# Optimization experiments

Hardware: AMD Instinct MI355X
Metric: run time of the kernel (lower is better)

## Reference

```python
import jax, jax.numpy as jnp
import numpy as np

T = 4096
HIDDEN = 2048
N_HEADS = 16
N_KV_HEADS = 4
HEAD_DIM = 128
WINDOW = 1024  # per_layer_sliding_window = WINDOW + 1 -> q attends keys with q_pos - k_pos <= WINDOW
ROPE_THETA = 100000.0
QKV_OUT = (N_HEADS + 2 * N_KV_HEADS) * HEAD_DIM  # 3072


def setup_inputs() -> dict:
    key = jax.random.key(0)
    k1, k2, k3, k4 = jax.random.split(key, 4)
    return {
        "hidden_states": jax.random.normal(k1, (T, HIDDEN), dtype=jnp.float32),
        "positions": jnp.arange(T, dtype=jnp.int32),
        "w_qkv": jax.random.normal(k2, (HIDDEN, QKV_OUT), dtype=jnp.float32) * 0.02,
        "b_qkv": jax.random.normal(k3, (QKV_OUT,), dtype=jnp.float32) * 0.02,
        "w_o": jax.random.normal(k4, (N_HEADS * HEAD_DIM, HIDDEN), dtype=jnp.float32) * 0.02,
    }


def _apply_rope(x, positions):
    # x: [T, n_heads, HEAD_DIM], neox-style rotary over full head dim
    half = HEAD_DIM // 2
    inv_freq = 1.0 / (ROPE_THETA ** (jnp.arange(half, dtype=jnp.float32) / half))
    freqs = positions.astype(jnp.float32)[:, None] * inv_freq[None, :]  # [T, half]
    cos = jnp.cos(freqs)[:, None, :]  # [T, 1, half]
    sin = jnp.sin(freqs)[:, None, :]
    x1, x2 = x[..., :half], x[..., half:]
    return jnp.concatenate([x1 * cos - x2 * sin, x2 * cos + x1 * sin], axis=-1)


def reference(hidden_states, positions, w_qkv, b_qkv, w_o):
    # QKV projection (bias=True)
    qkv = hidden_states @ w_qkv + b_qkv  # [T, QKV_OUT]
    q_size = N_HEADS * HEAD_DIM
    kv_size = N_KV_HEADS * HEAD_DIM
    q = qkv[:, :q_size].reshape(T, N_HEADS, HEAD_DIM)
    k = qkv[:, q_size:q_size + kv_size].reshape(T, N_KV_HEADS, HEAD_DIM)
    v = qkv[:, q_size + kv_size:].reshape(T, N_KV_HEADS, HEAD_DIM)

    # RoPE on q and k
    q = _apply_rope(q, positions)
    k = _apply_rope(k, positions)

    # GQA: expand kv heads to match query heads
    group = N_HEADS // N_KV_HEADS
    k = jnp.repeat(k, group, axis=1)  # [T, N_HEADS, HEAD_DIM]
    v = jnp.repeat(v, group, axis=1)

    scale = HEAD_DIM ** -0.5
    scores = jnp.einsum('qhd,khd->hqk', q, k) * scale  # [H, T, T]

    # causal + sliding-window mask: j <= i and i - j <= WINDOW
    i = jnp.arange(T)[:, None]
    j = jnp.arange(T)[None, :]
    mask = (j <= i) & (i - j <= WINDOW)  # [T, T]
    scores = jnp.where(mask[None, :, :], scores, jnp.finfo(scores.dtype).min)

    probs = jax.nn.softmax(scores, axis=-1)
    attn = jnp.einsum('hqk,khd->qhd', probs, v)  # [T, H, HEAD_DIM]
    attn = attn.reshape(T, N_HEADS * HEAD_DIM)

    # output projection (bias=False)
    return attn @ w_o
```

## Files before the change

kernel.cpp:

```cpp
#include <hip/hip_runtime.h>
#include <cstdint>

#define T_TOK 4096
#define HID 2048
#define NH 16
#define NKV 4
#define HD 128
#define WIN 1024
#define QKVO 3072

typedef float f32x4 __attribute__((ext_vector_type(4)));
typedef float f32x16 __attribute__((ext_vector_type(16)));
typedef __bf16 bf16x8 __attribute__((ext_vector_type(8)));
typedef __bf16 bf16x4 __attribute__((ext_vector_type(4)));
typedef unsigned int u32x4 __attribute__((ext_vector_type(4)));

__device__ __forceinline__ void gload16(const void* g, void* lds) {
  auto gp = reinterpret_cast<__attribute__((address_space(1))) void*>(
      reinterpret_cast<uintptr_t>(g));
  auto lp = reinterpret_cast<__attribute__((address_space(3))) void*>(
      reinterpret_cast<uintptr_t>(lds));
  __builtin_amdgcn_global_load_lds(gp, lp, 16, 0, 0);
}

__device__ __forceinline__ f32x4 mfma16(bf16x8 a, bf16x8 b, f32x4 c) {
  return __builtin_amdgcn_mfma_f32_16x16x32_bf16(a, b, c, 0, 0, 0);
}
__device__ __forceinline__ f32x16 mfma32(bf16x8 a, bf16x8 b, f32x16 c) {
  return __builtin_amdgcn_mfma_f32_32x32x16_bf16(a, b, c, 0, 0, 0);
}
__device__ __forceinline__ unsigned cvtpk(float lo, float hi) {
  unsigned r;
  asm("v_cvt_pk_bf16_f32 %0, %1, %2" : "=v"(r) : "v"(lo), "v"(hi));
  return r;
}
__device__ __forceinline__ void pl32swap(unsigned& a, unsigned& b) {
  asm volatile("v_permlane32_swap_b32 %0, %1" : "+v"(a), "+v"(b));
}

__global__ __launch_bounds__(256) void k_f32_to_bf16(const float* __restrict__ x,
                                                     __bf16* __restrict__ y) {
  const size_t e = (size_t)blockIdx.x * 256 + threadIdx.x;
  const float4* xv = (const float4*)x;
  float4 a = xv[e * 2], b = xv[e * 2 + 1];
  bf16x8 o;
  o[0] = (__bf16)a.x; o[1] = (__bf16)a.y; o[2] = (__bf16)a.z; o[3] = (__bf16)a.w;
  o[4] = (__bf16)b.x; o[5] = (__bf16)b.y; o[6] = (__bf16)b.z; o[7] = (__bf16)b.w;
  *(bf16x8*)(y + e * 8) = o;
}

__global__ __launch_bounds__(256) void k_transpose2(
    const float* __restrict__ W1, __bf16* __restrict__ Wt1,
    const float* __restrict__ W2, __bf16* __restrict__ Wt2) {
  __shared__ float lt[64][69];
  int bid = blockIdx.x;
  const float* W;
  __bf16* Wt;
  int R, C;
  if (bid < 1536) {
    W = W1; Wt = Wt1; R = HID; C = QKVO;
  } else {
    bid -= 1536; W = W2; Wt = Wt2; R = HID; C = HID;
  }
  const int nbx = C >> 6;
  const int c0 = (bid % nbx) << 6;
  const int r0 = (bid / nbx) << 6;
  const int tid = threadIdx.x;
  const int tx = tid & 15, ty = tid >> 4;
#pragma unroll
  for (int i = 0; i < 4; i++) {
    const int r = ty + 16 * i;
    const float4 v = *(const float4*)(W + (size_t)(r0 + r) * C + c0 + 4 * tx);
    lt[r][4 * tx] = v.x;
    lt[r][4 * tx + 1] = v.y;
    lt[r][4 * tx + 2] = v.z;
    lt[r][4 * tx + 3] = v.w;
  }
  __syncthreads();
  const int ux = tid & 7, uy = tid >> 3;
#pragma unroll
  for (int i = 0; i < 2; i++) {
    const int c = uy + 32 * i;
    bf16x8 o;
#pragma unroll
    for (int k = 0; k < 8; k++) o[k] = (__bf16)lt[8 * ux + k][c];
    *(bf16x8*)(Wt + (size_t)(c0 + c) * R + r0 + 8 * ux) = o;
  }
}

__global__ void k_rope_tab(const int* __restrict__ pos, float* __restrict__ cosT,
                           float* __restrict__ sinT) {
  const int t = blockIdx.x;
  const int d = threadIdx.x;
  const float inv = exp2f(-(float)d * (16.609640474436812f / 64.0f));
  const float fr = (float)pos[t] * inv;
  cosT[t * 64 + d] = cosf(fr);
  sinT[t * 64 + d] = sinf(fr);
}

template <int MODE>
__global__ __launch_bounds__(256, 2) void k_gemm(
    const __bf16* __restrict__ A, const __bf16* __restrict__ Bt,
    const float* __restrict__ bias, float* __restrict__ C,
    const float* __restrict__ cosT, const float* __restrict__ sinT,
    __bf16* __restrict__ Qp, __bf16* __restrict__ Kp, __bf16* __restrict__ Vf,
    int M, int N, int K) {
  __shared__ __align__(16) __bf16 smem[32768];
  const int tid = threadIdx.x;
  const int lane = tid & 63;
  const int w = tid >> 6;
  const int wr = w >> 1, wc = w & 1;
  const int c = lane & 15, g = lane >> 4;
  const int csw = (c & 7) << 4;

  const int nstc = N >> 9;
  const int bid = blockIdx.x;
  const int xcd = bid & 7;
  const int j = bid >> 3;
  const int spx = (int)(gridDim.x >> 7);
  const int s = xcd * spx + (j >> 4);
  const int q = j & 15;
  const int by = (s / nstc) * 4 + (q >> 2);
  const int bx = (s % nstc) * 4 + (q & 3);
  const int m0 = by << 7, n0 = bx << 7;

  const int o0 = w * 4096 + lane * 16;
  const int srow = 32 * w + (lane >> 3);
  const int schunk = (lane & 7) ^ ((lane >> 3) & 7);
  const __bf16* gA0 = A + (size_t)(m0 + srow) * K + schunk * 8;
  const __bf16* gB0 = Bt + (size_t)(n0 + srow) * K + schunk * 8;

  f32x4 acc[4][4] = {};

  {
    char* la = (char*)smem;
    char* lb = (char*)smem + 32768;
#pragma unroll
    for (int qq = 0; qq < 4; qq++) {
      gload16(gA0 + (size_t)qq * 8 * K, la + o0 + qq * 1024);
      gload16(gB0 + (size_t)qq * 8 * K, lb + o0 + qq * 1024);
    }
  }
  __syncthreads();

  int cur = 0;
  for (int kt = 0; kt < K; kt += 64) {
    if (kt + 64 < K) {
      char* la = (char*)smem + (cur ^ 1) * 16384;
      char* lb = (char*)smem + 32768 + (cur ^ 1) * 16384;
#pragma unroll
      for (int qq = 0; qq < 4; qq++) {
        gload16(gA0 + kt + 64 + (size_t)qq * 8 * K, la + o0 + qq * 1024);
        gload16(gB0 + kt + 64 + (size_t)qq * 8 * K, lb + o0 + qq * 1024);
      }
    }
    const char* as = (const char*)smem + cur * 16384;
    const char* bs = (const char*)smem + 32768 + cur * 16384;
#pragma unroll
    for (int ds = 0; ds < 2; ds++) {
      bf16x8 af[4], bfr[4];
#pragma unroll
      for (int mi = 0; mi < 4; mi++)
        af[mi] = *(const bf16x8*)(as + (wr * 64 + mi * 16 + c) * 128 +
                                  ((ds * 64 + g * 16) ^ csw));
#pragma unroll
      for (int ni = 0; ni < 4; ni++)
        bfr[ni] = *(const bf16x8*)(bs + (wc * 64 + ni * 16 + c) * 128 +
                                   ((ds * 64 + g * 16) ^ csw));
#pragma unroll
      for (int mi = 0; mi < 4; mi++)
#pragma unroll
        for (int ni = 0; ni < 4; ni++)
          acc[mi][ni] = mfma16(af[mi], bfr[ni], acc[mi][ni]);
    }
    __syncthreads();
    cur ^= 1;
  }

  if constexpr (MODE == 0) {
#pragma unroll
    for (int ni = 0; ni < 4; ni++) {
      const int col = n0 + wc * 64 + ni * 16 + c;
#pragma unroll
      for (int mi = 0; mi < 4; mi++)
#pragma unroll
        for (int r = 0; r < 4; r++) {
          const int row = m0 + wr * 64 + mi * 16 + 4 * g + r;
          C[(size_t)row * N + col] = acc[mi][ni][r];
        }
    }
  } else {
    __bf16* sm = smem;
#pragma unroll
    for (int ni = 0; ni < 4; ni++) {
      const int col = wc * 64 + ni * 16 + c;
      const float bv = bias[n0 + col];
#pragma unroll
      for (int mi = 0; mi < 4; mi++)
#pragma unroll
        for (int r = 0; r < 4; r++)
          sm[(wr * 64 + mi * 16 + 4 * g + r) * 136 + col] =
              (__bf16)(acc[mi][ni][r] + bv);
    }
    __syncthreads();

    if (n0 < (NH + NKV) * HD) {
      const bool isq = n0 < NH * HD;
      const float sc = isq ? (0.08838834764831845f * 1.4426950408889634f) : 1.0f;
      __bf16* base = isq ? (Qp + (size_t)(n0 >> 7) * T_TOK * HD)
                         : (Kp + (size_t)((n0 >> 7) - NH) * T_TOK * HD);
#pragma unroll
      for (int jj = 0; jj < 4; jj++) {
        const int e = jj * 256 + tid;
        const int tl = e >> 3, ch = e & 7;
        const int tt = m0 + tl;
        const bf16x8 x1 = *(const bf16x8*)(sm + tl * 136 + ch * 8);
        const bf16x8 x2 = *(const bf16x8*)(sm + tl * 136 + 64 + ch * 8);
        const float4 c0 = *(const float4*)(cosT + tt * 64 + ch * 8);
        const float4 c1 = *(const float4*)(cosT + tt * 64 + ch * 8 + 4);
        const float4 s0 = *(const float4*)(sinT + tt * 64 + ch * 8);
        const float4 s1 = *(const float4*)(sinT + tt * 64 + ch * 8 + 4);
        const float cs[8] = {c0.x, c0.y, c0.z, c0.w, c1.x, c1.y, c1.z, c1.w};
        const float sn[8] = {s0.x, s0.y, s0.z, s0.w, s1.x, s1.y, s1.z, s1.w};
        bf16x8 o1, o2;
#pragma unroll
        for (int i = 0; i < 8; i++) {
          const float a = (float)x1[i], b = (float)x2[i];
          o1[i] = (__bf16)((a * cs[i] - b * sn[i]) * sc);
          o2[i] = (__bf16)((b * cs[i] + a * sn[i]) * sc);
        }
        const int d2s = isq ? ch * 8 : ((ch * 8) ^ ((tt & 7) << 3));
        __bf16* dst = base + (size_t)tt * HD;
        *(bf16x8*)(dst + d2s) = o1;
        *(bf16x8*)(dst + 64 + d2s) = o2;
      }
    } else {
      const int kv = (n0 >> 7) - (NH + NKV);
#pragma unroll
      for (int st2 = 0; st2 < 2; st2++) {
        __bf16* outb = Vf + ((size_t)kv * 64 + (m0 >> 6) + st2) * 8192;
#pragma unroll
        for (int jj = 0; jj < 4; jj++) {
          const int u = jj * 256 + tid;
          const int lu = u & 63, ks = (u >> 6) & 3, mq = u >> 8;
          const int d = mq * 32 + (lu & 31);
          const int tb = st2 * 64 + ks * 16 + ((lu >> 5) << 3);
          bf16x8 o;
#pragma unroll
          for (int jz = 0; jz < 8; jz++) o[jz] = sm[(tb + jz) * 136 + d];
          *(bf16x8*)(outb + (size_t)u * 8) = o;
        }
      }
    }
  }
}

__global__ __launch_bounds__(256, 2) void k_attn(const __bf16* __restrict__ Qp,
                                                 const __bf16* __restrict__ Kp,
                                                 const __bf16* __restrict__ Vf,
                                                 __bf16* __restrict__ attnO) {
  __shared__ __align__(16) __bf16 Ks[2][64 * 128];

  const int tid = threadIdx.x;
  const int lane = tid & 63;
  const int w = tid >> 6;
  const int l31 = lane & 31;
  const int hi = lane >> 5;
  const int swz = (lane & 7) << 4;
  const int bid = blockIdx.x;
  const int xcd = bid & 7, j = bid >> 3;
  const int h = ((xcd >> 1) << 2) + ((xcd & 1) << 1) + (j & 1);
  const int qb = 31 - (j >> 1);
  const int kvh = h >> 2;
  const int q0 = qb * 128;
  const int iw = q0 + 32 * w;
  const int irow = iw + l31;

  bf16x8 qf[8];
  {
    const __bf16* qbase = Qp + ((size_t)h * T_TOK + irow) * HD;
#pragma unroll
    for (int ds = 0; ds < 8; ds++)
      qf[ds] = *(const bf16x8*)(qbase + ds * 16 + hi * 8);
  }

  f32x16 ot[4] = {};
  float mrun = 0.0f, lrun = 0.0f;

  const int jstart = (q0 >= WIN) ? (q0 - WIN) : 0;
  const int niter = (q0 + 128 - jstart) >> 6;

  const char* Kg = (const char*)Kp + (size_t)kvh * T_TOK * HD * 2;
  const char* kg0 = Kg + (size_t)(jstart + 16 * w + (lane >> 4)) * 256 + (lane & 15) * 16;
  const __bf16* Vgb = Vf + (size_t)kvh * 64 * 8192;

#pragma unroll
  for (int q = 0; q < 4; q++)
    gload16(kg0 + q * 1024, (char*)&Ks[0][0] + w * 4096 + q * 1024);

  int cur = 0;

  for (int it = 0; it < niter; ++it) {
    const int j0 = jstart + it * 64;
    __syncthreads();

    if (it + 1 < niter) {
      const char* kg = kg0 + (size_t)(it + 1) * 16384;
      char* kd = (char*)&Ks[cur ^ 1][0] + w * 4096;
#pragma unroll
      for (int q = 0; q < 4; q++) gload16(kg + q * 1024, kd + q * 1024);
    }

    if (j0 > iw + 31) { cur ^= 1; continue; }
    if (iw - (j0 + 63) > WIN) { cur ^= 1; continue; }

    const __bf16* vt = Vgb + (size_t)(j0 >> 6) * 8192;
    bf16x8 vf[4][4];
#pragma unroll
    for (int m = 0; m < 4; m++)
#pragma unroll
      for (int ks = 0; ks < 4; ks++)
        vf[m][ks] = *(const bf16x8*)(vt + (m * 256 + ks * 64 + lane) * 8);

    const char* kb = (const char*)&Ks[cur][0];

    f32x16 st[2] = {};
    __builtin_amdgcn_s_setprio(1);
#pragma unroll
    for (int t = 0; t < 2; t++)
#pragma unroll
      for (int ds = 0; ds < 8; ds++) {
        bf16x8 kf = *(const bf16x8*)(kb + (t * 32 + l31) * 256 +
                                     ((ds * 32 + hi * 16) ^ swz));
        st[t] = mfma32(kf, qf[ds], st[t]);
      }
    __builtin_amdgcn_s_setprio(0);

    float p[2][16];
    float cmax = -1e30f;
    const bool interior = (j0 + 63 <= iw) && (iw + 31 - j0 <= WIN);
    if (interior) {
#pragma unroll
      for (int t = 0; t < 2; t++)
#pragma unroll
        for (int r = 0; r < 16; r++) {
          const float s = st[t][r];
          p[t][r] = s;
          cmax = fmaxf(cmax, s);
        }
    } else {
      const int jb = irow - j0 - 4 * hi;
#pragma unroll
      for (int t = 0; t < 2; t++)
#pragma unroll
        for (int r = 0; r < 16; r++) {
          float s = st[t][r];
          const int off = 32 * t + (r & 3) + 8 * (r >> 2);
          s = ((unsigned)(jb - off) <= WIN) ? s : -1e30f;
          p[t][r] = s;
          cmax = fmaxf(cmax, s);
        }
    }
    cmax = fmaxf(cmax, __shfl_xor(cmax, 32));

    if (!__all(cmax <= mrun + 11.54f)) {
      const float mn = fmaxf(mrun, cmax);
      const float alpha = exp2f(mrun - mn);
      lrun *= alpha;
#pragma unroll
      for (int m = 0; m < 4; m++) ot[m] *= alpha;
      mrun = mn;
    }
    float rs = 0.0f;
#pragma unroll
    for (int t = 0; t < 2; t++)
#pragma unroll
      for (int r = 0; r < 16; r++) {
        const float e_ = exp2f(p[t][r] - mrun);
        p[t][r] = e_;
        rs += e_;
      }
    rs += __shfl_xor(rs, 32);
    lrun += rs;

    bf16x8 pb[4];
#pragma unroll
    for (int t = 0; t < 2; t++) {
      unsigned wds[8];
#pragma unroll
      for (int i = 0; i < 8; i++) wds[i] = cvtpk(p[t][2 * i], p[t][2 * i + 1]);
      pl32swap(wds[0], wds[2]);
      pl32swap(wds[1], wds[3]);
      pl32swap(wds[4], wds[6]);
      pl32swap(wds[5], wds[7]);
      u32x4 f0 = {wds[0], wds[1], wds[2], wds[3]};
      u32x4 f1 = {wds[4], wds[5], wds[6], wds[7]};
      pb[2 * t] = __builtin_bit_cast(bf16x8, f0);
      pb[2 * t + 1] = __builtin_bit_cast(bf16x8, f1);
    }

    __builtin_amdgcn_s_setprio(1);
#pragma unroll
    for (int m = 0; m < 4; m++)
#pragma unroll
      for (int ks = 0; ks < 4; ks++)
        ot[m] = mfma32(vf[m][ks], pb[ks], ot[m]);
    __builtin_amdgcn_s_setprio(0);

    cur ^= 1;
  }

  const float inv_l = 1.0f / lrun;
  __bf16* orow = attnO + (size_t)irow * (NH * HD) + h * HD;
#pragma unroll
  for (int m = 0; m < 4; m++)
#pragma unroll
    for (int rg = 0; rg < 4; rg++) {
      const int d0 = 32 * m + 8 * rg + 4 * hi;
      bf16x4 o4;
#pragma unroll
      for (int r = 0; r < 4; r++) o4[r] = (__bf16)(ot[m][4 * rg + r] * inv_l);
      *(bf16x4*)(orow + d0) = o4;
    }
}

extern "C" void kernel_launch(void* const* d_in, const int* in_sizes, int n_in,
                              void* d_out, int out_size, void* d_ws, size_t ws_size,
                              hipStream_t stream) {
  (void)in_sizes; (void)n_in; (void)out_size; (void)ws_size;
  const float* hidden = (const float*)d_in[0];
  const int* positions = (const int*)d_in[1];
  const float* w_qkv = (const float*)d_in[2];
  const float* b_qkv = (const float*)d_in[3];
  const float* w_o = (const float*)d_in[4];
  float* out = (float*)d_out;

  char* ws = (char*)d_ws;
  __bf16* Hb = (__bf16*)ws;    ws += (size_t)T_TOK * HID * 2;
  __bf16* Wqkvt = (__bf16*)ws; ws += (size_t)QKVO * HID * 2;
  __bf16* Wot = (__bf16*)ws;   ws += (size_t)HID * HID * 2;
  float* cosT = (float*)ws;    ws += (size_t)T_TOK * 64 * 4;
  float* sinT = (float*)ws;    ws += (size_t)T_TOK * 64 * 4;
  __bf16* Qp = (__bf16*)ws;    ws += (size_t)NH * T_TOK * HD * 2;
  __bf16* Kp = (__bf16*)ws;    ws += (size_t)NKV * T_TOK * HD * 2;
  __bf16* Vfb = (__bf16*)ws;   ws += (size_t)NKV * 64 * 8192 * 2;
  __bf16* attnb = (__bf16*)ws; ws += (size_t)T_TOK * NH * HD * 2;

  k_f32_to_bf16<<<T_TOK * HID / (256 * 8), 256, 0, stream>>>(hidden, Hb);
  k_transpose2<<<2560, 256, 0, stream>>>(w_qkv, Wqkvt, w_o, Wot);
  k_rope_tab<<<T_TOK, 64, 0, stream>>>(positions, cosT, sinT);
  k_gemm<1><<<(T_TOK / 128) * (QKVO / 128), 256, 0, stream>>>(
      Hb, Wqkvt, b_qkv, nullptr, cosT, sinT, Qp, Kp, Vfb, T_TOK, QKVO, HID);
  k_attn<<<512, 256, 0, stream>>>(Qp, Kp, Vfb, attnb);
  k_gemm<0><<<(T_TOK / 128) * (HID / 128), 256, 0, stream>>>(
      attnb, Wot, nullptr, out, nullptr, nullptr, nullptr, nullptr, nullptr,
      T_TOK, HID, HID);
}
```

Measured before the change: 172.4 us.

## Store K in MFMA-fragment layout and load directly to registers in attention

The QKV GEMM epilogue now writes roped K into a pre-swizzled per-64-token fragment layout, the same way V is stored, so each lane's MFMA operand is one contiguous 16-byte load. The attention kernel drops the shared-memory K double buffer and its per-iteration barriers and reads K fragments straight from global/L2. Each wave also iterates only over its own 32-row key range instead of the block-wide range, which removes idle iterations. The cost is more global load traffic per wave, with no shared-memory reuse of K across the four waves, and higher register pressure from holding 16 K fragments.

```diff
diff --git a/kernel.cpp b/kernel.cpp
--- a/kernel.cpp
+++ b/kernel.cpp
@@ -103,7 +103,7 @@
     const __bf16* __restrict__ A, const __bf16* __restrict__ Bt,
     const float* __restrict__ bias, float* __restrict__ C,
     const float* __restrict__ cosT, const float* __restrict__ sinT,
-    __bf16* __restrict__ Qp, __bf16* __restrict__ Kp, __bf16* __restrict__ Vf,
+    __bf16* __restrict__ Qp, __bf16* __restrict__ Kf, __bf16* __restrict__ Vf,
     int M, int N, int K) {
   __shared__ __align__(16) __bf16 smem[32768];
   const int tid = threadIdx.x;
@@ -204,11 +204,9 @@
     }
     __syncthreads();
 
-    if (n0 < (NH + NKV) * HD) {
-      const bool isq = n0 < NH * HD;
-      const float sc = isq ? (0.08838834764831845f * 1.4426950408889634f) : 1.0f;
-      __bf16* base = isq ? (Qp + (size_t)(n0 >> 7) * T_TOK * HD)
-                         : (Kp + (size_t)((n0 >> 7) - NH) * T_TOK * HD);
+    if (n0 < NH * HD) {
+      const float sc = 0.08838834764831845f * 1.4426950408889634f;
+      __bf16* base = Qp + (size_t)(n0 >> 7) * T_TOK * HD;
 #pragma unroll
       for (int jj = 0; jj < 4; jj++) {
         const int e = jj * 256 + tid;
@@ -229,10 +227,49 @@
           o1[i] = (__bf16)((a * cs[i] - b * sn[i]) * sc);
           o2[i] = (__bf16)((b * cs[i] + a * sn[i]) * sc);
         }
-        const int d2s = isq ? ch * 8 : ((ch * 8) ^ ((tt & 7) << 3));
         __bf16* dst = base + (size_t)tt * HD;
-        *(bf16x8*)(dst + d2s) = o1;
-        *(bf16x8*)(dst + 64 + d2s) = o2;
+        *(bf16x8*)(dst + ch * 8) = o1;
+        *(bf16x8*)(dst + 64 + ch * 8) = o2;
+      }
+    } else if (n0 < (NH + NKV) * HD) {
+#pragma unroll
+      for (int jj = 0; jj < 4; jj++) {
+        const int e = jj * 256 + tid;
+        const int tl = e >> 3, ch = e & 7;
+        const int tt = m0 + tl;
+        const bf16x8 x1 = *(const bf16x8*)(sm + tl * 136 + ch * 8);
+        const bf16x8 x2 = *(const bf16x8*)(sm + tl * 136 + 64 + ch * 8);
+        const float4 c0 = *(const float4*)(cosT + tt * 64 + ch * 8);
+        const float4 c1 = *(const float4*)(cosT + tt * 64 + ch * 8 + 4);
+        const float4 s0 = *(const float4*)(sinT + tt * 64 + ch * 8);
+        const float4 s1 = *(const float4*)(sinT + tt * 64 + ch * 8 + 4);
+        const float cs[8] = {c0.x, c0.y, c0.z, c0.w, c1.x, c1.y, c1.z, c1.w};
+        const float sn[8] = {s0.x, s0.y, s0.z, s0.w, s1.x, s1.y, s1.z, s1.w};
+        bf16x8 o1, o2;
+#pragma unroll
+        for (int i = 0; i < 8; i++) {
+          const float a = (float)x1[i], b = (float)x2[i];
+          o1[i] = (__bf16)(a * cs[i] - b * sn[i]);
+          o2[i] = (__bf16)(b * cs[i] + a * sn[i]);
+        }
+        *(bf16x8*)(sm + tl * 136 + ch * 8) = o1;
+        *(bf16x8*)(sm + tl * 136 + 64 + ch * 8) = o2;
+      }
+      __syncthreads();
+      const int kvidx = (n0 >> 7) - NH;
+#pragma unroll
+      for (int st2 = 0; st2 < 2; st2++) {
+        __bf16* outb = Kf + ((size_t)kvidx * 64 + (m0 >> 6) + st2) * 8192;
+#pragma unroll
+        for (int jj = 0; jj < 4; jj++) {
+          const int u = jj * 256 + tid;
+          const int lu = u & 63, un = u >> 6;
+          const int t2 = un >> 3, ds = un & 7;
+          const int row = st2 * 64 + t2 * 32 + (lu & 31);
+          const int kcol = ds * 16 + ((lu >> 5) << 3);
+          const bf16x8 o = *(const bf16x8*)(sm + row * 136 + kcol);
+          *(bf16x8*)(outb + (size_t)u * 8) = o;
+        }
       }
     } else {
       const int kv = (n0 >> 7) - (NH + NKV);
@@ -256,17 +293,14 @@
 }
 
 __global__ __launch_bounds__(256, 2) void k_attn(const __bf16* __restrict__ Qp,
-                                                 const __bf16* __restrict__ Kp,
+                                                 const __bf16* __restrict__ Kf,
                                                  const __bf16* __restrict__ Vf,
                                                  __bf16* __restrict__ attnO) {
-  __shared__ __align__(16) __bf16 Ks[2][64 * 128];
-
   const int tid = threadIdx.x;
   const int lane = tid & 63;
   const int w = tid >> 6;
   const int l31 = lane & 31;
   const int hi = lane >> 5;
-  const int swz = (lane & 7) << 4;
   const int bid = blockIdx.x;
   const int xcd = bid & 7, j = bid >> 3;
   const int h = ((xcd >> 1) << 2) + ((xcd & 1) << 1) + (j & 1);
@@ -287,53 +321,36 @@
   f32x16 ot[4] = {};
   float mrun = 0.0f, lrun = 0.0f;
 
-  const int jstart = (q0 >= WIN) ? (q0 - WIN) : 0;
-  const int niter = (q0 + 128 - jstart) >> 6;
-
-  const char* Kg = (const char*)Kp + (size_t)kvh * T_TOK * HD * 2;
-  const char* kg0 = Kg + (size_t)(jstart + 16 * w + (lane >> 4)) * 256 + (lane & 15) * 16;
+  const int t0i = (iw >= WIN) ? ((iw - WIN) >> 6) : 0;
+  const int t1i = (iw + 31) >> 6;
+  const __bf16* Kgb = Kf + (size_t)kvh * 64 * 8192;
   const __bf16* Vgb = Vf + (size_t)kvh * 64 * 8192;
 
-#pragma unroll
-  for (int q = 0; q < 4; q++)
-    gload16(kg0 + q * 1024, (char*)&Ks[0][0] + w * 4096 + q * 1024);
-
-  int cur = 0;
-
-  for (int it = 0; it < niter; ++it) {
-    const int j0 = jstart + it * 64;
-    __syncthreads();
-
-    if (it + 1 < niter) {
-      const char* kg = kg0 + (size_t)(it + 1) * 16384;
-      char* kd = (char*)&Ks[cur ^ 1][0] + w * 4096;
-#pragma unroll
-      for (int q = 0; q < 4; q++) gload16(kg + q * 1024, kd + q * 1024);
-    }
-
-    if (j0 > iw + 31) { cur ^= 1; continue; }
-    if (iw - (j0 + 63) > WIN) { cur ^= 1; continue; }
-
-    const __bf16* vt = Vgb + (size_t)(j0 >> 6) * 8192;
+  for (int tt = t0i; tt <= t1i; ++tt) {
+    const int j0 = tt * 64;
+    const __bf16* kt = Kgb + (size_t)tt * 8192;
+    const __bf16* vt = Vgb + (size_t)tt * 8192;
+
+    bf16x8 kfA[8], kfB[8];
+#pragma unroll
+    for (int ds = 0; ds < 8; ds++)
+      kfA[ds] = *(const bf16x8*)(kt + (size_t)(ds * 64 + lane) * 8);
+#pragma unroll
+    for (int ds = 0; ds < 8; ds++)
+      kfB[ds] = *(const bf16x8*)(kt + (size_t)((8 + ds) * 64 + lane) * 8);
     bf16x8 vf[4][4];
 #pragma unroll
     for (int m = 0; m < 4; m++)
 #pragma unroll
       for (int ks = 0; ks < 4; ks++)
-        vf[m][ks] = *(const bf16x8*)(vt + (m * 256 + ks * 64 + lane) * 8);
-
-    const char* kb = (const char*)&Ks[cur][0];
+        vf[m][ks] = *(const bf16x8*)(vt + (size_t)(m * 256 + ks * 64 + lane) * 8);
 
     f32x16 st[2] = {};
     __builtin_amdgcn_s_setprio(1);
 #pragma unroll
-    for (int t = 0; t < 2; t++)
-#pragma unroll
-      for (int ds = 0; ds < 8; ds++) {
-        bf16x8 kf = *(const bf16x8*)(kb + (t * 32 + l31) * 256 +
-                                     ((ds * 32 + hi * 16) ^ swz));
-        st[t] = mfma32(kf, qf[ds], st[t]);
-      }
+    for (int ds = 0; ds < 8; ds++) st[0] = mfma32(kfA[ds], qf[ds], st[0]);
+#pragma unroll
+    for (int ds = 0; ds < 8; ds++) st[1] = mfma32(kfB[ds], qf[ds], st[1]);
     __builtin_amdgcn_s_setprio(0);
 
     float p[2][16];
@@ -406,8 +423,6 @@
       for (int ks = 0; ks < 4; ks++)
         ot[m] = mfma32(vf[m][ks], pb[ks], ot[m]);
     __builtin_amdgcn_s_setprio(0);
-
-    cur ^= 1;
   }
 
   const float inv_l = 1.0f / lrun;
@@ -442,7 +457,7 @@
   float* cosT = (float*)ws;    ws += (size_t)T_TOK * 64 * 4;
   float* sinT = (float*)ws;    ws += (size_t)T_TOK * 64 * 4;
   __bf16* Qp = (__bf16*)ws;    ws += (size_t)NH * T_TOK * HD * 2;
-  __bf16* Kp = (__bf16*)ws;    ws += (size_t)NKV * T_TOK * HD * 2;
+  __bf16* Kfb = (__bf16*)ws;   ws += (size_t)NKV * 64 * 8192 * 2;
   __bf16* Vfb = (__bf16*)ws;   ws += (size_t)NKV * 64 * 8192 * 2;
   __bf16* attnb = (__bf16*)ws; ws += (size_t)T_TOK * NH * HD * 2;
 
@@ -450,8 +465,8 @@
   k_transpose2<<<2560, 256, 0, stream>>>(w_qkv, Wqkvt, w_o, Wot);
   k_rope_tab<<<T_TOK, 64, 0, stream>>>(positions, cosT, sinT);
   k_gemm<1><<<(T_TOK / 128) * (QKVO / 128), 256, 0, stream>>>(
-      Hb, Wqkvt, b_qkv, nullptr, cosT, sinT, Qp, Kp, Vfb, T_TOK, QKVO, HID);
-  k_attn<<<512, 256, 0, stream>>>(Qp, Kp, Vfb, attnb);
+      Hb, Wqkvt, b_qkv, nullptr, cosT, sinT, Qp, Kfb, Vfb, T_TOK, QKVO, HID);
+  k_attn<<<512, 256, 0, stream>>>(Qp, Kfb, Vfb, attnb);
   k_gemm<0><<<(T_TOK / 128) * (HID / 128), 256, 0, stream>>>(
       attnb, Wot, nullptr, out, nullptr, nullptr, nullptr, nullptr, nullptr,
       T_TOK, HID, HID);
```

Result: slower. 192.9 us (+11.9%).
